# Kernel optimization log

Hardware: AMD Instinct MI355X
Metric: run time of the kernel (lower is better)

The kernel has to match this reference:

```python
import jax, jax.numpy as jnp
import numpy as np

NMS_PRE, NMS_POST, NMS_THRESH = 1024, 512, 0.7
B, A, FEAT = 4, 70400, 27648
BN_EPS = 1e-5


def _bev_iou(boxes):
    # boxes: [K, 7] (x, y, z, dx, dy, dz, ry); axis-aligned BEV IoU
    x, y, dx, dy = boxes[:, 0], boxes[:, 1], boxes[:, 3], boxes[:, 4]
    x1, x2 = x - 0.5 * dx, x + 0.5 * dx
    y1, y2 = y - 0.5 * dy, y + 0.5 * dy
    iw = jnp.clip(jnp.minimum(x2[:, None], x2[None, :]) - jnp.maximum(x1[:, None], x1[None, :]), 0.0)
    ih = jnp.clip(jnp.minimum(y2[:, None], y2[None, :]) - jnp.maximum(y1[:, None], y1[None, :]), 0.0)
    inter = iw * ih
    area = dx * dy
    return inter / jnp.clip(area[:, None] + area[None, :] - inter, 1e-6)


def _greedy_nms(boxes, thresh):
    # boxes sorted by score desc; returns keep mask [K]
    K = boxes.shape[0]
    iou = _bev_iou(boxes)
    idx = jnp.arange(K)

    def step(keep, i):
        sup = (iou[i] > thresh) & (idx > i) & keep[i]
        return keep & ~sup, None

    keep, _ = jax.lax.scan(step, jnp.ones(K, dtype=bool), jnp.arange(K))
    return keep


def _proposal_one(box, cls):
    # box: [A, 7], cls: [A, n_cls]  ->  padded rois [NPOST,7], scores [NPOST], labels [NPOST]
    score = jnp.max(cls, axis=-1)
    label = jnp.argmax(cls, axis=-1)
    top_score, top_idx = jax.lax.top_k(score, NMS_PRE)
    top_box = box[top_idx]
    keep = _greedy_nms(top_box, NMS_THRESH)
    # stable: kept entries first, preserving score order
    order = jnp.argsort(jnp.where(keep, jnp.arange(NMS_PRE), NMS_PRE + jnp.arange(NMS_PRE)))
    sel = order[:NMS_POST]
    valid = jnp.arange(NMS_POST) < jnp.minimum(jnp.sum(keep), NMS_POST)
    rois = jnp.where(valid[:, None], top_box[sel], 0.0)
    roi_score = jnp.where(valid, top_score[sel], 0.0)
    roi_label = jnp.where(valid, label[top_idx][sel], 0) + 1  # +1 as in module
    return rois, roi_score, roi_label


def _bn_relu(h, g, b):
    # eval-mode BN with running_mean=0, running_var=1
    return jax.nn.relu(h * (g / jnp.sqrt(1.0 + BN_EPS)) + b)


def _decode(reg, anchors):
    # ResidualCoder_v1.decode_torch
    xa, ya, za = anchors[..., 0], anchors[..., 1], anchors[..., 2]
    dxa, dya, dza, ra = anchors[..., 3], anchors[..., 4], anchors[..., 5], anchors[..., 6]
    xt, yt, zt = reg[..., 0], reg[..., 1], reg[..., 2]
    dxt, dyt, dzt, rt = reg[..., 3], reg[..., 4], reg[..., 5], reg[..., 6]
    diag = jnp.sqrt(dxa * dxa + dya * dya)
    return jnp.stack([
        xt * diag + xa, yt * diag + ya, zt * dza + za,
        jnp.exp(dxt) * dxa, jnp.exp(dyt) * dya, jnp.exp(dzt) * dza,
        rt + ra], axis=-1)


def _rotate_z(box, ang):
    # rotate x,y of box [..., 7] by ang [...]
    c, s = jnp.cos(ang), jnp.sin(ang)
    x = box[..., 0] * c - box[..., 1] * s
    y = box[..., 0] * s + box[..., 1] * c
    return jnp.concatenate([x[..., None], y[..., None], box[..., 2:]], axis=-1)


def reference(rpn_box_preds, rpn_cls_preds, pooled_features,
              Ws1, g1, b1, Ws2, g2, b2,
              Wc1, gc1, bc1, Wc2, gc2, bc2, Wc3, bc3,
              Wr1, gr1, br1, Wr2, gr2, br2, Wr3, br3):
    # proposal_layer: per-batch topk + NMS + padded scatter (vmapped)
    rois, roi_scores, roi_labels = jax.vmap(_proposal_one)(rpn_box_preds, rpn_cls_preds)

    # shared / cls / reg heads (1x1 Conv1d == per-roi MLP), dropout off (eval)
    x = _bn_relu(pooled_features @ Ws1.T, g1, b1)
    x = _bn_relu(x @ Ws2.T, g2, b2)
    c = _bn_relu(x @ Wc1.T, gc1, bc1)
    c = _bn_relu(c @ Wc2.T, gc2, bc2)
    cls_preds = c @ Wc3.T + bc3          # [B*NPOST, 1]
    r = _bn_relu(x @ Wr1.T, gr1, br1)
    r = _bn_relu(r @ Wr2.T, gr2, br2)
    reg_preds = r @ Wr3.T + br3          # [B*NPOST, 7]

    bsz = rois.shape[0]
    cls_preds = cls_preds.reshape(bsz, -1, cls_preds.shape[-1])
    reg_preds = reg_preds.reshape(bsz, -1, 7)

    # generate_predict_box: decode against detached rois with xyz zeroed
    anchors = jax.lax.stop_gradient(rois)
    anchors = anchors.at[..., 0:3].set(0.0)
    box_ct = _decode(reg_preds, anchors)
    box_preds = _rotate_z(box_ct, rois[..., 6])
    box_preds = jnp.concatenate([box_preds[..., 0:3] + rois[..., 0:3], box_preds[..., 3:]], axis=-1)

    return jnp.concatenate([cls_preds, box_preds, roi_scores[..., None]], axis=-1)  # [B, NPOST, 9]


def setup_inputs():
    key = jax.random.key(0)
    ks = jax.random.split(key, 32)
    u = jax.random.uniform(ks[0], (B, A, 7), dtype=jnp.float32)
    lo = jnp.array([0.0, -40.0, -2.0, 1.5, 1.4, 1.0, -3.14159], jnp.float32)
    hi = jnp.array([70.0, 40.0, 0.0, 4.5, 2.0, 2.0, 3.14159], jnp.float32)
    rpn_box_preds = lo + u * (hi - lo)
    rpn_cls_preds = jax.random.normal(ks[1], (B, A, 3), dtype=jnp.float32)
    pooled_features = jax.random.normal(ks[2], (B * NMS_POST, FEAT), dtype=jnp.float32) * 0.1

    def w(k, o, i, std=None):
        s = (1.0 / np.sqrt(i)) if std is None else std
        return jax.random.normal(k, (o, i), dtype=jnp.float32) * s

    d = dict(
        rpn_box_preds=rpn_box_preds, rpn_cls_preds=rpn_cls_preds, pooled_features=pooled_features,
        Ws1=w(ks[3], 256, FEAT), g1=jnp.ones(256), b1=jnp.zeros(256),
        Ws2=w(ks[4], 256, 256), g2=jnp.ones(256), b2=jnp.zeros(256),
        Wc1=w(ks[5], 256, 256), gc1=jnp.ones(256), bc1=jnp.zeros(256),
        Wc2=w(ks[6], 256, 256), gc2=jnp.ones(256), bc2=jnp.zeros(256),
        Wc3=w(ks[7], 1, 256), bc3=jnp.zeros(1),
        Wr1=w(ks[8], 256, 256), gr1=jnp.ones(256), br1=jnp.zeros(256),
        Wr2=w(ks[9], 256, 256), gr2=jnp.ones(256), br2=jnp.zeros(256),
        Wr3=w(ks[10], 7, 256, std=0.001), br3=jnp.zeros(7),
    )
    return d
```

## Files before the change

### kernel.cpp

```cpp
#include <hip/hip_runtime.h>
#include <cstdint>

typedef unsigned int u32;
typedef unsigned long long u64;
typedef unsigned short u16;

#define BATCH 4
#define A_CNT 70400
#define FEAT 27648
#define KSPLIT 16
#define KCHUNK 1728
#define NTILE_IT 27

typedef __attribute__((ext_vector_type(8))) short bf16x8;
typedef __attribute__((ext_vector_type(4))) float f32x4;
typedef __attribute__((ext_vector_type(4))) u32 u32x4;

constexpr size_t OF_KEYS = 0;
constexpr size_t OF_TBOX = OF_KEYS + 1126400;
constexpr size_t OF_TSC  = OF_TBOX + 114688;
constexpr size_t OF_BX1  = OF_TSC + 16384;
constexpr size_t OF_BX2  = OF_BX1 + 16384;
constexpr size_t OF_BY1  = OF_BX2 + 16384;
constexpr size_t OF_BY2  = OF_BY1 + 16384;
constexpr size_t OF_BAR  = OF_BY2 + 16384;
constexpr size_t OF_MASK = OF_BAR + 16384;
constexpr size_t OF_ROIS = OF_MASK + 524288;
constexpr size_t OF_RSC  = OF_ROIS + 57344;
constexpr size_t OF_BSW  = OF_RSC + 8192;
constexpr size_t OF_PART = OF_BSW + 14155776;
constexpr size_t WS_NEED = OF_PART + 33554432;

__device__ __forceinline__ u32 keyOf(float f) {
  u32 u = __float_as_uint(f);
  return (u & 0x80000000u) ? ~u : (u | 0x80000000u);
}
__device__ __forceinline__ float keyToF(u32 k) {
  u32 u = (k & 0x80000000u) ? (k ^ 0x80000000u) : ~k;
  return __uint_as_float(u);
}
__device__ __forceinline__ u16 f2bf(float f) {
  u32 u = __float_as_uint(f);
  u32 r = 0x7FFFu + ((u >> 16) & 1u);
  return (u16)((u + r) >> 16);
}
__device__ __forceinline__ void gload_lds16(const void* g, void* l) {
  auto gp = reinterpret_cast<const __attribute__((address_space(1))) unsigned int*>(
      reinterpret_cast<uintptr_t>(g));
  auto lp = reinterpret_cast<__attribute__((address_space(3))) unsigned int*>(
      reinterpret_cast<uintptr_t>(l));
  __builtin_amdgcn_global_load_lds(gp, lp, 16, 0, 0);
}
__device__ __forceinline__ u64 shflx64(u64 v, int m) {
  u32 lo = (u32)v, hi = (u32)(v >> 32);
  lo = __shfl_xor(lo, m, 64);
  hi = __shfl_xor(hi, m, 64);
  return ((u64)hi << 32) | lo;
}

__global__ __launch_bounds__(1024) void k_fatA(const float* __restrict__ cls,
    const float* __restrict__ Ws1, u32* __restrict__ keys, u32* __restrict__ Bsw)
{
  int bid = blockIdx.x;
  int t = threadIdx.x;
  if (bid < 864) {
    u32 w = (u32)bid * 1024u + t;
    u32 tile = w >> 11;
    u32 rem = w & 2047u;
    u32 n = rem >> 3;
    u32 pq = (rem & 7u) << 4;
    u32 q0 = pq ^ ((n & 7u) << 4);
    u32 col0 = tile * 64u + (q0 >> 1);
    const float* src = Ws1 + (size_t)n * FEAT + col0;
    float4 f0 = *(const float4*)src;
    float4 f1 = *(const float4*)(src + 4);
    u32x4 o;
    o.x = (u32)f2bf(f0.x) | ((u32)f2bf(f0.y) << 16);
    o.y = (u32)f2bf(f0.z) | ((u32)f2bf(f0.w) << 16);
    o.z = (u32)f2bf(f1.x) | ((u32)f2bf(f1.y) << 16);
    o.w = (u32)f2bf(f1.z) | ((u32)f2bf(f1.w) << 16);
    ((u32x4*)Bsw)[w] = o;
    return;
  }
  u32 g = (u32)(bid - 864) * 1024u + t;
  float s0 = cls[(size_t)g * 3 + 0];
  float s1 = cls[(size_t)g * 3 + 1];
  float s2 = cls[(size_t)g * 3 + 2];
  keys[g] = keyOf(fmaxf(s0, fmaxf(s1, s2)));
}

__global__ __launch_bounds__(1024) void k_prop(const u32* __restrict__ keys,
    const float* __restrict__ boxes, float* __restrict__ tbox, float* __restrict__ tsc,
    float* __restrict__ bx1, float* __restrict__ bx2, float* __restrict__ by1,
    float* __restrict__ by2, float* __restrict__ bar)
{
  int b = blockIdx.x, t = threadIdx.x;
  int lane = t & 63, wv = t >> 6;
  const u32* kb = keys + (size_t)b * A_CNT;
  __shared__ u64 s[2048];
  __shared__ u32 partials[16];
  __shared__ u32 cc;
  u32 h[35];
#pragma unroll
  for (int j = 0; j < 35; ++j) {
    int g0 = t + ((2 * j) << 10);
    int g1 = t + ((2 * j + 1) << 10);
    u32 a = (g0 < A_CNT) ? (kb[g0] >> 16) : 0u;
    u32 c2 = (g1 < A_CNT) ? (kb[g1] >> 16) : 0u;
    h[j] = a | (c2 << 16);
  }
  if (t == 0) cc = 0u;
  u32 lo = 0, hi = 65536;
  while (hi - lo > 1) {
    u32 mid = (lo + hi) >> 1;
    u32 c = 0;
#pragma unroll
    for (int j = 0; j < 35; ++j) {
      c += ((h[j] & 0xFFFFu) >= mid) ? 1u : 0u;
      c += ((h[j] >> 16) >= mid) ? 1u : 0u;
    }
#pragma unroll
    for (int o = 32; o > 0; o >>= 1) c += __shfl_xor(c, o, 64);
    __syncthreads();
    if (lane == 0) partials[wv] = c;
    __syncthreads();
    u32 tot = 0;
#pragma unroll
    for (int w2 = 0; w2 < 16; ++w2) tot += partials[w2];
    if (tot >= 1024u) lo = mid; else hi = mid;
  }
  u32 kth = lo;
  __syncthreads();
#pragma unroll 1
  for (int i = 0; i < 69; ++i) {
    int g = t + (i << 10);
    u32 k = (g < A_CNT) ? kb[g] : 0u;
    bool pass = (g < A_CNT) && ((k >> 16) >= kth);
    u64 mm = __ballot(pass);
    if (mm) {
      int leader = __ffsll((unsigned long long)mm) - 1;
      u32 base = 0;
      if (lane == leader) base = atomicAdd(&cc, (u32)__popcll(mm));
      base = __shfl(base, leader, 64);
      if (pass) {
        u32 pos = base + (u32)__popcll(mm & ((1ull << lane) - 1ull));
        if (pos < 2048u) s[pos] = ((u64)k << 32) | (u32)(~(u32)g);
      }
    }
  }
  __syncthreads();
  u32 m = cc; if (m > 2048u) m = 2048u;
  for (int e = t; e < 2048; e += 1024) if (e >= (int)m) s[e] = 0ull;
  __syncthreads();
  {
    u64 v0 = s[2 * t], v1 = s[2 * t + 1];
#pragma unroll
    for (u32 k = 2; k <= 128; k <<= 1) {
      bool desc = ((t & (k >> 1)) == 0);
#pragma unroll
      for (u32 j = (k >> 1); j >= 2; j >>= 1) {
        u32 mmk = j >> 1;
        u64 p0 = shflx64(v0, mmk);
        u64 p1 = shflx64(v1, mmk);
        bool up = ((t & mmk) == 0);
        bool mx = (desc == up);
        v0 = mx ? (v0 > p0 ? v0 : p0) : (v0 < p0 ? v0 : p0);
        v1 = mx ? (v1 > p1 ? v1 : p1) : (v1 < p1 ? v1 : p1);
      }
      if (desc ? (v0 < v1) : (v0 > v1)) { u64 tmp = v0; v0 = v1; v1 = tmp; }
    }
    s[2 * t] = v0; s[2 * t + 1] = v1;
    __syncthreads();
    for (u32 k = 256; k <= 2048; k <<= 1) {
      for (u32 j = k >> 1; j >= 128; j >>= 1) {
        for (int e = t; e < 2048; e += 1024) {
          u32 p = (u32)e ^ j;
          if (p > (u32)e) {
            bool d2 = ((e & k) == 0);
            u64 x = s[e], y = s[p];
            if (d2 ? (x < y) : (x > y)) { s[e] = y; s[p] = x; }
          }
        }
        __syncthreads();
      }
      u64 v0 = s[2 * t], v1 = s[2 * t + 1];
      bool desc = ((t & (k >> 1)) == 0);
#pragma unroll
      for (u32 j = 64; j >= 2; j >>= 1) {
        u32 mmk = j >> 1;
        u64 p0 = shflx64(v0, mmk);
        u64 p1 = shflx64(v1, mmk);
        bool up = ((t & mmk) == 0);
        bool mx = (desc == up);
        v0 = mx ? (v0 > p0 ? v0 : p0) : (v0 < p0 ? v0 : p0);
        v1 = mx ? (v1 > p1 ? v1 : p1) : (v1 < p1 ? v1 : p1);
      }
      if (desc ? (v0 < v1) : (v0 > v1)) { u64 tmp = v0; v0 = v1; v1 = tmp; }
      s[2 * t] = v0; s[2 * t + 1] = v1;
      __syncthreads();
    }
  }
  u64 comp = s[t];
  u32 kk = (u32)(comp >> 32);
  u32 a = ~(u32)(comp & 0xFFFFFFFFull);
  int o = b * 1024 + t;
  tsc[o] = keyToF(kk);
  const float* bp = boxes + ((size_t)b * A_CNT + a) * 7;
  float x = bp[0], y = bp[1], z = bp[2], dx = bp[3], dy = bp[4], dz = bp[5], rr = bp[6];
  float* tb = tbox + (size_t)o * 7;
  tb[0] = x; tb[1] = y; tb[2] = z; tb[3] = dx; tb[4] = dy; tb[5] = dz; tb[6] = rr;
  {
#pragma clang fp contract(off)
    bx1[o] = x - 0.5f * dx; bx2[o] = x + 0.5f * dx;
    by1[o] = y - 0.5f * dy; by2[o] = y + 0.5f * dy;
    bar[o] = dx * dy;
  }
}

__global__ __launch_bounds__(256) void k_fatB(const float* __restrict__ A,
    const u32* __restrict__ Bsw, float* __restrict__ part,
    const float* __restrict__ bx1, const float* __restrict__ bx2,
    const float* __restrict__ by1, const float* __restrict__ by2,
    const float* __restrict__ bar, u32* __restrict__ mask)
{
  __shared__ u32x4 Alds4[64 * 8];
  __shared__ u32x4 Blds4[256 * 8];
  int bid = blockIdx.x;
  if (bid >= 512) {
    int mi = bid - 512;
    int b = mi >> 6;
    int cbk = (mi >> 2) & 15;
    int rb0 = (mi & 3) * 4;
    int tt = threadIdx.x;
    int rbi = tt >> 6, ln = tt & 63;
    int r = (rb0 + rbi) * 64 + ln;
    int o = b * 1024, jc0 = cbk * 64;
    __shared__ float cx1[64], cx2[64], cy1[64], cy2[64], car[64];
    if (tt < 64) {
      cx1[tt] = bx1[o + jc0 + tt]; cx2[tt] = bx2[o + jc0 + tt];
      cy1[tt] = by1[o + jc0 + tt]; cy2[tt] = by2[o + jc0 + tt];
      car[tt] = bar[o + jc0 + tt];
    }
    __syncthreads();
    float rx1 = bx1[o + r], rx2 = bx2[o + r], ry1 = by1[o + r], ry2 = by2[o + r], rar = bar[o + r];
    u32 w0 = 0, w1 = 0;
    {
#pragma clang fp contract(off)
      for (int c = 0; c < 64; ++c) {
        int jc = jc0 + c;
        float iw = fminf(rx2, cx2[c]) - fmaxf(rx1, cx1[c]); iw = fmaxf(iw, 0.0f);
        float ih = fminf(ry2, cy2[c]) - fmaxf(ry1, cy1[c]); ih = fmaxf(ih, 0.0f);
        float inter = iw * ih;
        float den = fmaxf(rar + car[c] - inter, 1e-6f);
        float iou = inter / den;
        if ((iou > 0.7f) && (jc > r)) {
          if (c < 32) w0 |= 1u << c; else w1 |= 1u << (c - 32);
        }
      }
    }
    mask[((size_t)(o + r)) * 32 + cbk * 2 + 0] = w0;
    mask[((size_t)(o + r)) * 32 + cbk * 2 + 1] = w1;
    return;
  }
  char* Alds = (char*)Alds4;
  char* Blds = (char*)Blds4;
  int q = bid >> 3;
  int ks = (bid & 7) * 2 + (q >> 5);
  int mt = q & 31;
  int tid = threadIdx.x, lane = tid & 63, wv = tid >> 6;

  f32x4 acc[4][4];
#pragma unroll
  for (int i = 0; i < 4; ++i)
#pragma unroll
    for (int j = 0; j < 4; ++j) acc[i][j] = (f32x4){0.f, 0.f, 0.f, 0.f};

  int am = tid >> 2;
  int ak = (tid & 3) * 16;
  const float* ap_base = A + ((size_t)(mt * 64 + am)) * FEAT + (size_t)ks * KCHUNK + ak;
  int asw = (am & 7) << 4;
  int ac0 = (tid & 3) * 32;
  char* aw0 = Alds + am * 128 + ((ac0) ^ asw);
  char* aw1 = Alds + am * 128 + ((ac0 + 16) ^ asw);
  const char* bsrc_base = (const char*)Bsw + ((size_t)(ks * NTILE_IT)) * 32768 + (wv * 8) * 1024 + lane * 16;
  char* bdst_base = Blds + (wv * 8) * 1024;

  int row16 = lane & 15, kgrp = lane >> 4;
  int aoff[4][2], boff[4][2];
#pragma unroll
  for (int ksub = 0; ksub < 2; ++ksub) {
    int qq = ksub * 64 + kgrp * 16;
#pragma unroll
    for (int mf = 0; mf < 4; ++mf) {
      int row = mf * 16 + row16;
      aoff[mf][ksub] = row * 128 + (qq ^ ((row & 7) << 4));
    }
#pragma unroll
    for (int nf = 0; nf < 4; ++nf) {
      int n = wv * 64 + nf * 16 + row16;
      boff[nf][ksub] = n * 128 + (qq ^ ((n & 7) << 4));
    }
  }

  for (int it = 0; it < NTILE_IT; ++it) {
    const float4* ap = (const float4*)(ap_base + it * 64);
    float4 f0 = ap[0], f1 = ap[1], f2 = ap[2], f3 = ap[3];
    u32x4 c0, c1;
    c0.x = (u32)f2bf(f0.x) | ((u32)f2bf(f0.y) << 16);
    c0.y = (u32)f2bf(f0.z) | ((u32)f2bf(f0.w) << 16);
    c0.z = (u32)f2bf(f1.x) | ((u32)f2bf(f1.y) << 16);
    c0.w = (u32)f2bf(f1.z) | ((u32)f2bf(f1.w) << 16);
    c1.x = (u32)f2bf(f2.x) | ((u32)f2bf(f2.y) << 16);
    c1.y = (u32)f2bf(f2.z) | ((u32)f2bf(f2.w) << 16);
    c1.z = (u32)f2bf(f3.x) | ((u32)f2bf(f3.y) << 16);
    c1.w = (u32)f2bf(f3.z) | ((u32)f2bf(f3.w) << 16);
    *(u32x4*)aw0 = c0;
    *(u32x4*)aw1 = c1;
    const char* bs = bsrc_base + (size_t)it * 32768;
#pragma unroll
    for (int i = 0; i < 8; ++i) gload_lds16(bs + i * 1024, bdst_base + i * 1024);
    __syncthreads();
    bf16x8 af[4][2], bfv[4][2];
#pragma unroll
    for (int ksub = 0; ksub < 2; ++ksub) {
#pragma unroll
      for (int mf = 0; mf < 4; ++mf) af[mf][ksub] = *(const bf16x8*)(Alds + aoff[mf][ksub]);
#pragma unroll
      for (int nf = 0; nf < 4; ++nf) bfv[nf][ksub] = *(const bf16x8*)(Blds + boff[nf][ksub]);
    }
#pragma unroll
    for (int ksub = 0; ksub < 2; ++ksub)
#pragma unroll
      for (int mf = 0; mf < 4; ++mf)
#pragma unroll
        for (int nf = 0; nf < 4; ++nf)
          acc[mf][nf] = __builtin_amdgcn_mfma_f32_16x16x32_bf16(af[mf][ksub], bfv[nf][ksub], acc[mf][nf], 0, 0, 0);
    __syncthreads();
  }
  float* pb = part + (size_t)ks * 524288;
#pragma unroll
  for (int mf = 0; mf < 4; ++mf) {
    int row = mt * 64 + mf * 16 + kgrp * 4;
#pragma unroll
    for (int nf = 0; nf < 4; ++nf) {
      int col = wv * 64 + nf * 16 + row16;
#pragma unroll
      for (int rr = 0; rr < 4; ++rr)
        pb[(size_t)(row + rr) * 256 + col] = acc[mf][nf][rr];
    }
  }
}

__global__ __launch_bounds__(64) void k_nms(const u32* __restrict__ mask,
    const float* __restrict__ tbox, const float* __restrict__ tsc,
    float* __restrict__ rois, float* __restrict__ rsc)
{
  int b = blockIdx.x;
  int lane = threadIdx.x;
  int el = lane & 31;
  const u32* M = mask + (size_t)b * 1024 * 32;
  u32 R = 0;
  u32 cur[32], nxt[32];
#pragma unroll
  for (int i = 0; i < 32; ++i) cur[i] = M[(size_t)(i * 32 + el)];
#pragma unroll 1
  for (int c = 0; c < 32; ++c) {
    if (c < 31) {
      int nb = (c + 1) * 1024 + el;
#pragma unroll
      for (int i = 0; i < 32; ++i) nxt[i] = M[(size_t)(nb + i * 32)];
    }
    u32 w = R;
#pragma unroll
    for (int i = 0; i < 32; ++i) w |= ((w >> i) & 1u) ? 0u : cur[i];
    u32 wfin = __shfl(w, c, 64);
#pragma unroll
    for (int i = 0; i < 32; ++i) R |= ((wfin >> i) & 1u) ? 0u : cur[i];
#pragma unroll
    for (int i = 0; i < 32; ++i) cur[i] = nxt[i];
  }
  u32 keepw = (lane < 32) ? ~R : 0u;
  int c = __popc(keepw);
  int pre = c;
  for (int d = 1; d < 64; d <<= 1) {
    int v = __shfl_up(pre, d, 64);
    if (lane >= d) pre += v;
  }
  int total = __shfl(pre, 31, 64);
  int base = pre - c;
  if (lane < 32) {
    u32 w = keepw;
    int rank = base;
    while (w) {
      int bit = __ffs(w) - 1;
      w &= w - 1;
      if (rank < 512) {
        int r = lane * 32 + bit;
        const float* tb = tbox + ((size_t)b * 1024 + r) * 7;
        float* rp = rois + ((size_t)b * 512 + rank) * 7;
        rp[0] = tb[0]; rp[1] = tb[1]; rp[2] = tb[2]; rp[3] = tb[3];
        rp[4] = tb[4]; rp[5] = tb[5]; rp[6] = tb[6];
        rsc[b * 512 + rank] = tsc[b * 1024 + r];
      }
      rank++;
    }
  }
  for (int z = total + lane; z < 512; z += 64) {
    float* rp = rois + ((size_t)b * 512 + z) * 7;
    rp[0] = rp[1] = rp[2] = rp[3] = rp[4] = rp[5] = rp[6] = 0.0f;
    rsc[b * 512 + z] = 0.0f;
  }
}

__device__ __forceinline__ void layer4(const float (*IN)[256], const float* __restrict__ W,
    const float* __restrict__ g, const float* __restrict__ bb, float (*OUT)[256], int t, int h)
{
  float acc[4] = {0, 0, 0, 0};
  const float* Wrow = W + (size_t)t * 256;
  for (int k = 0; k < 256; k += 4) {
    float4 w4 = *(const float4*)&Wrow[k];
#pragma unroll
    for (int r = 0; r < 4; ++r) {
      float4 xv = *(const float4*)&IN[h * 4 + r][k];
      acc[r] = fmaf(xv.x, w4.x, acc[r]);
      acc[r] = fmaf(xv.y, w4.y, acc[r]);
      acc[r] = fmaf(xv.z, w4.z, acc[r]);
      acc[r] = fmaf(xv.w, w4.w, acc[r]);
    }
  }
  float sc = g[t] / sqrtf(1.0f + 1e-5f);
  float bv = bb[t];
#pragma unroll
  for (int r = 0; r < 4; ++r)
    OUT[h * 4 + r][t] = fmaxf(fmaf(acc[r], sc, bv), 0.0f);
}

__global__ __launch_bounds__(512) void k_chain(const float* __restrict__ part,
    const float* __restrict__ Ws2, const float* __restrict__ Wc1, const float* __restrict__ Wc2,
    const float* __restrict__ Wr1, const float* __restrict__ Wr2,
    const float* __restrict__ g1, const float* __restrict__ b1,
    const float* __restrict__ g2, const float* __restrict__ b2,
    const float* __restrict__ gc1, const float* __restrict__ bc1,
    const float* __restrict__ gc2, const float* __restrict__ bc2,
    const float* __restrict__ gr1, const float* __restrict__ br1,
    const float* __restrict__ gr2, const float* __restrict__ br2,
    const float* __restrict__ Wc3, const float* __restrict__ bc3,
    const float* __restrict__ Wr3, const float* __restrict__ br3,
    const float* __restrict__ rois, const float* __restrict__ rsc,
    float* __restrict__ out)
{
  int bid = blockIdx.x, tid = threadIdx.x;
  int t = tid & 255, h = tid >> 8;
  __shared__ __align__(16) float bufX[8][256];
  __shared__ __align__(16) float bufY[8][256];
  __shared__ __align__(16) float bufC[8][256];
  __shared__ __align__(16) float bufR[8][256];
  __shared__ float hd[64];
  {
    float sc = g1[t] / sqrtf(1.0f + 1e-5f);
    float bv = b1[t];
#pragma unroll
    for (int r = 0; r < 4; ++r) {
      int row = h * 4 + r;
      float s = 0.f;
#pragma unroll
      for (int ks = 0; ks < KSPLIT; ++ks)
        s += part[(size_t)ks * 524288 + (size_t)(bid * 8 + row) * 256 + t];
      bufX[row][t] = fmaxf(fmaf(s, sc, bv), 0.0f);
    }
  }
  __syncthreads();
  layer4(bufX, Ws2, g2, b2, bufY, t, h);
  __syncthreads();
  layer4(bufY, Wc1, gc1, bc1, bufC, t, h);
  layer4(bufY, Wr1, gr1, br1, bufR, t, h);
  __syncthreads();
  layer4(bufC, Wc2, gc2, bc2, bufX, t, h);
  layer4(bufR, Wr2, gr2, br2, bufY, t, h);
  __syncthreads();
  int wv = tid >> 6, ln = tid & 63;
  for (int task = wv; task < 64; task += 8) {
    float p;
    if (task < 8) {
      float4 yv = *(const float4*)&bufX[task][ln * 4];
      float4 w4 = ((const float4*)Wc3)[ln];
      p = yv.x * w4.x + yv.y * w4.y + yv.z * w4.z + yv.w * w4.w;
    } else {
      int i = task - 8, row = i / 7, j = i % 7;
      float4 yv = *(const float4*)&bufY[row][ln * 4];
      float4 w4 = ((const float4*)(Wr3 + j * 256))[ln];
      p = yv.x * w4.x + yv.y * w4.y + yv.z * w4.z + yv.w * w4.w;
    }
#pragma unroll
    for (int off = 32; off > 0; off >>= 1) p += __shfl_xor(p, off, 64);
    if (ln == 0) hd[task] = p;
  }
  __syncthreads();
  if (tid < 8) {
    int m = bid * 8 + tid;
    float clsv = hd[tid] + bc3[0];
    float rg[7];
#pragma unroll
    for (int j = 0; j < 7; ++j) rg[j] = hd[8 + tid * 7 + j] + br3[j];
    const float* R = rois + (size_t)m * 7;
    float rx = R[0], ry = R[1], rz = R[2], dxa = R[3], dya = R[4], dza = R[5], ra = R[6];
    float diag = sqrtf(dxa * dxa + dya * dya);
    float x = rg[0] * diag, y = rg[1] * diag, z = rg[2] * dza;
    float ex = expf(rg[3]) * dxa, ey = expf(rg[4]) * dya, ez = expf(rg[5]) * dza;
    float hr = rg[6] + ra;
    float cc = cosf(ra), sn = sinf(ra);
    float xr = x * cc - y * sn, yr = x * sn + y * cc;
    float* O = out + (size_t)m * 9;
    O[0] = clsv; O[1] = xr + rx; O[2] = yr + ry; O[3] = z + rz;
    O[4] = ex; O[5] = ey; O[6] = ez; O[7] = hr; O[8] = rsc[m];
  }
}

extern "C" void kernel_launch(void* const* d_in, const int* in_sizes, int n_in,
                              void* d_out, int out_size, void* d_ws, size_t ws_size,
                              hipStream_t stream)
{
  const float* rpn_box = (const float*)d_in[0];
  const float* rpn_cls = (const float*)d_in[1];
  const float* pooled  = (const float*)d_in[2];
  const float* Ws1 = (const float*)d_in[3];
  const float* g1  = (const float*)d_in[4];
  const float* b1  = (const float*)d_in[5];
  const float* Ws2 = (const float*)d_in[6];
  const float* g2  = (const float*)d_in[7];
  const float* b2  = (const float*)d_in[8];
  const float* Wc1 = (const float*)d_in[9];
  const float* gc1 = (const float*)d_in[10];
  const float* bc1 = (const float*)d_in[11];
  const float* Wc2 = (const float*)d_in[12];
  const float* gc2 = (const float*)d_in[13];
  const float* bc2 = (const float*)d_in[14];
  const float* Wc3 = (const float*)d_in[15];
  const float* bc3 = (const float*)d_in[16];
  const float* Wr1 = (const float*)d_in[17];
  const float* gr1 = (const float*)d_in[18];
  const float* br1 = (const float*)d_in[19];
  const float* Wr2 = (const float*)d_in[20];
  const float* gr2 = (const float*)d_in[21];
  const float* br2 = (const float*)d_in[22];
  const float* Wr3 = (const float*)d_in[23];
  const float* br3 = (const float*)d_in[24];

  if (ws_size < WS_NEED) return;

  char* ws = (char*)d_ws;
  u32* keys = (u32*)(ws + OF_KEYS);
  float* tbox = (float*)(ws + OF_TBOX);
  float* tsc  = (float*)(ws + OF_TSC);
  float* bx1 = (float*)(ws + OF_BX1);
  float* bx2 = (float*)(ws + OF_BX2);
  float* by1 = (float*)(ws + OF_BY1);
  float* by2 = (float*)(ws + OF_BY2);
  float* bar = (float*)(ws + OF_BAR);
  u32* mask = (u32*)(ws + OF_MASK);
  float* roisb = (float*)(ws + OF_ROIS);
  float* rscb  = (float*)(ws + OF_RSC);
  u32* Bsw = (u32*)(ws + OF_BSW);
  float* part = (float*)(ws + OF_PART);

  k_fatA<<<1139, 1024, 0, stream>>>(rpn_cls, Ws1, keys, Bsw);
  k_prop<<<4, 1024, 0, stream>>>(keys, rpn_box, tbox, tsc, bx1, bx2, by1, by2, bar);
  k_fatB<<<768, 256, 0, stream>>>(pooled, Bsw, part, bx1, bx2, by1, by2, bar, mask);
  k_nms<<<4, 64, 0, stream>>>(mask, tbox, tsc, roisb, rscb);
  k_chain<<<256, 512, 0, stream>>>(part, Ws2, Wc1, Wc2, Wr1, Wr2,
                                   g1, b1, g2, b2, gc1, bc1, gc2, bc2,
                                   gr1, br1, gr2, br2, Wc3, bc3, Wr3, br3,
                                   roisb, rscb, (float*)d_out);
}
```

Measured before the change: 269.6 us.

## Double-buffer GEMM tiles in LDS and prefetch key loads in top-k scan

The split-K GEMM in the fat kernel now keeps two LDS buffers for the A and B tiles. The next tile's global loads and async B copies are issued before the current tile's MFMAs, and its bf16 conversion and store happen after them, so one barrier per iteration replaces two. The top-k compaction loop also software-prefetches the next key value. The cost is LDS use growing to 80KB per block, which may cut occupancy, plus extra registers for the prefetched floats.

```diff
diff --git a/kernel.cpp b/kernel.cpp
--- a/kernel.cpp
+++ b/kernel.cpp
@@ -131,10 +131,15 @@
   }
   u32 kth = lo;
   __syncthreads();
+  u32 kc = kb[t];
 #pragma unroll 1
   for (int i = 0; i < 69; ++i) {
     int g = t + (i << 10);
-    u32 k = (g < A_CNT) ? kb[g] : 0u;
+    u32 k = kc;
+    if (i < 68) {
+      int gn = t + ((i + 1) << 10);
+      kc = (gn < A_CNT) ? kb[gn] : 0u;
+    }
     bool pass = (g < A_CNT) && ((k >> 16) >= kth);
     u64 mm = __ballot(pass);
     if (mm) {
@@ -223,8 +228,7 @@
     const float* __restrict__ by1, const float* __restrict__ by2,
     const float* __restrict__ bar, u32* __restrict__ mask)
 {
-  __shared__ u32x4 Alds4[64 * 8];
-  __shared__ u32x4 Blds4[256 * 8];
+  __shared__ __align__(16) char smem[81920];
   int bid = blockIdx.x;
   if (bid >= 512) {
     int mi = bid - 512;
@@ -235,7 +239,11 @@
     int rbi = tt >> 6, ln = tt & 63;
     int r = (rb0 + rbi) * 64 + ln;
     int o = b * 1024, jc0 = cbk * 64;
-    __shared__ float cx1[64], cx2[64], cy1[64], cy2[64], car[64];
+    float* cx1 = (float*)(smem);
+    float* cx2 = (float*)(smem + 256);
+    float* cy1 = (float*)(smem + 512);
+    float* cy2 = (float*)(smem + 768);
+    float* car = (float*)(smem + 1024);
     if (tt < 64) {
       cx1[tt] = bx1[o + jc0 + tt]; cx2[tt] = bx2[o + jc0 + tt];
       cy1[tt] = by1[o + jc0 + tt]; cy2[tt] = by2[o + jc0 + tt];
@@ -262,8 +270,6 @@
     mask[((size_t)(o + r)) * 32 + cbk * 2 + 1] = w1;
     return;
   }
-  char* Alds = (char*)Alds4;
-  char* Blds = (char*)Blds4;
   int q = bid >> 3;
   int ks = (bid & 7) * 2 + (q >> 5);
   int mt = q & 31;
@@ -280,10 +286,10 @@
   const float* ap_base = A + ((size_t)(mt * 64 + am)) * FEAT + (size_t)ks * KCHUNK + ak;
   int asw = (am & 7) << 4;
   int ac0 = (tid & 3) * 32;
-  char* aw0 = Alds + am * 128 + ((ac0) ^ asw);
-  char* aw1 = Alds + am * 128 + ((ac0 + 16) ^ asw);
+  int awoff0 = am * 128 + (ac0 ^ asw);
+  int awoff1 = am * 128 + ((ac0 + 16) ^ asw);
   const char* bsrc_base = (const char*)Bsw + ((size_t)(ks * NTILE_IT)) * 32768 + (wv * 8) * 1024 + lane * 16;
-  char* bdst_base = Blds + (wv * 8) * 1024;
+  int bdoff = (wv * 8) * 1024;
 
   int row16 = lane & 15, kgrp = lane >> 4;
   int aoff[4][2], boff[4][2];
@@ -302,8 +308,8 @@
     }
   }
 
-  for (int it = 0; it < NTILE_IT; ++it) {
-    const float4* ap = (const float4*)(ap_base + it * 64);
+  {
+    const float4* ap = (const float4*)ap_base;
     float4 f0 = ap[0], f1 = ap[1], f2 = ap[2], f3 = ap[3];
     u32x4 c0, c1;
     c0.x = (u32)f2bf(f0.x) | ((u32)f2bf(f0.y) << 16);
@@ -314,19 +320,37 @@
     c1.y = (u32)f2bf(f2.z) | ((u32)f2bf(f2.w) << 16);
     c1.z = (u32)f2bf(f3.x) | ((u32)f2bf(f3.y) << 16);
     c1.w = (u32)f2bf(f3.z) | ((u32)f2bf(f3.w) << 16);
-    *(u32x4*)aw0 = c0;
-    *(u32x4*)aw1 = c1;
-    const char* bs = bsrc_base + (size_t)it * 32768;
-#pragma unroll
-    for (int i = 0; i < 8; ++i) gload_lds16(bs + i * 1024, bdst_base + i * 1024);
-    __syncthreads();
+    *(u32x4*)(smem + awoff0) = c0;
+    *(u32x4*)(smem + awoff1) = c1;
+#pragma unroll
+    for (int i = 0; i < 8; ++i)
+      gload_lds16(bsrc_base + i * 1024, smem + 16384 + bdoff + i * 1024);
+  }
+  __syncthreads();
+
+  for (int it = 0; it < NTILE_IT; ++it) {
+    int cur = it & 1;
+    char* Acur = smem + (cur ? 8192 : 0);
+    char* Bcur = smem + 16384 + (cur ? 32768 : 0);
+    char* Anxt = smem + (cur ? 0 : 8192);
+    char* Bnxt = smem + 16384 + (cur ? 0 : 32768);
+    bool has = (it + 1 < NTILE_IT);
+    float4 f0n, f1n, f2n, f3n;
+    if (has) {
+      const float4* ap = (const float4*)(ap_base + (it + 1) * 64);
+      f0n = ap[0]; f1n = ap[1]; f2n = ap[2]; f3n = ap[3];
+      const char* bs = bsrc_base + (size_t)(it + 1) * 32768;
+#pragma unroll
+      for (int i = 0; i < 8; ++i)
+        gload_lds16(bs + i * 1024, Bnxt + bdoff + i * 1024);
+    }
     bf16x8 af[4][2], bfv[4][2];
 #pragma unroll
     for (int ksub = 0; ksub < 2; ++ksub) {
 #pragma unroll
-      for (int mf = 0; mf < 4; ++mf) af[mf][ksub] = *(const bf16x8*)(Alds + aoff[mf][ksub]);
-#pragma unroll
-      for (int nf = 0; nf < 4; ++nf) bfv[nf][ksub] = *(const bf16x8*)(Blds + boff[nf][ksub]);
+      for (int mf = 0; mf < 4; ++mf) af[mf][ksub] = *(const bf16x8*)(Acur + aoff[mf][ksub]);
+#pragma unroll
+      for (int nf = 0; nf < 4; ++nf) bfv[nf][ksub] = *(const bf16x8*)(Bcur + boff[nf][ksub]);
     }
 #pragma unroll
     for (int ksub = 0; ksub < 2; ++ksub)
@@ -335,6 +359,19 @@
 #pragma unroll
         for (int nf = 0; nf < 4; ++nf)
           acc[mf][nf] = __builtin_amdgcn_mfma_f32_16x16x32_bf16(af[mf][ksub], bfv[nf][ksub], acc[mf][nf], 0, 0, 0);
+    if (has) {
+      u32x4 c0, c1;
+      c0.x = (u32)f2bf(f0n.x) | ((u32)f2bf(f0n.y) << 16);
+      c0.y = (u32)f2bf(f0n.z) | ((u32)f2bf(f0n.w) << 16);
+      c0.z = (u32)f2bf(f1n.x) | ((u32)f2bf(f1n.y) << 16);
+      c0.w = (u32)f2bf(f1n.z) | ((u32)f2bf(f1n.w) << 16);
+      c1.x = (u32)f2bf(f2n.x) | ((u32)f2bf(f2n.y) << 16);
+      c1.y = (u32)f2bf(f2n.z) | ((u32)f2bf(f2n.w) << 16);
+      c1.z = (u32)f2bf(f3n.x) | ((u32)f2bf(f3n.y) << 16);
+      c1.w = (u32)f2bf(f3n.z) | ((u32)f2bf(f3n.w) << 16);
+      *(u32x4*)(Anxt + awoff0) = c0;
+      *(u32x4*)(Anxt + awoff1) = c1;
+    }
     __syncthreads();
   }
   float* pb = part + (size_t)ks * 524288;
```

After: 259.7 us. -3.7%, faster.
